# Kernel optimization log

Measured on AMD Instinct MI355X. Metric: run time of the kernel, lower is better.

The kernel has to match this reference:

```python
import jax, jax.numpy as jnp
import numpy as np

B, S, D, R = 2, 2048, 1024, 224  # batch, seq, n_embd, table_size


def setup_inputs() -> dict:
    key = jax.random.key(0)
    k = jax.random.split(key, 6)
    return {
        "hidden_states": jax.random.normal(k[0], (B, S, D), jnp.float32),
        "w_row": jax.random.normal(k[1], (D, R), jnp.float32) * 0.02,
        "b_row": jnp.zeros((R,), jnp.float32),
        "col_weight": jax.random.normal(k[2], (R, D, R), jnp.float32) * 0.02,
        "col_bias": jnp.zeros((R, R), jnp.float32),
        "target_row_ids": jax.random.randint(k[3], (B, S), 0, R, jnp.int32),
        "target_col_ids": jax.random.randint(k[4], (B, S), 0, R, jnp.int32),
    }


def reference(hidden_states, w_row, b_row, col_weight, col_bias,
              target_row_ids, target_col_ids):
    Bv, Sv, Dv = hidden_states.shape
    Rv = col_bias.shape[0]
    N = Bv * Sv
    hs_flat = hidden_states.reshape(N, Dv)
    r = target_row_ids.reshape(N)
    c = target_col_ids.reshape(N)

    # row loss: standard cross entropy over table_size row logits (mean)
    row_logits = hs_flat @ w_row + b_row                      # [N, R]
    logp_row = jax.nn.log_softmax(row_logits, axis=-1)
    loss_row = -jnp.take_along_axis(logp_row, r[:, None].astype(jnp.int32), axis=1)[:, 0].mean()

    # column loss: per-token row-routed projection + cross entropy (sum / N).
    # Mathematically identical to the original per-row masked loop: each token
    # uses col_weight[row_id] / col_bias[row_id]. We process tokens in fixed-size
    # chunks with lax.scan so FLOPs match the original (N*D*R, not N*R*D*R) and
    # the gathered per-token weights stay bounded in memory.
    CHUNK = 256  # N = 4096 divisible by CHUNK
    hs_c = hs_flat.reshape(N // CHUNK, CHUNK, Dv)
    r_c = r.reshape(N // CHUNK, CHUNK)
    c_c = c.reshape(N // CHUNK, CHUNK)

    def body(acc, xs):
        h, ri, ci = xs                          # [C,D], [C], [C]
        w = col_weight[ri]                      # [C, D, R] irregular gather
        b = col_bias[ri]                        # [C, R]
        logits = jnp.einsum('cd,cdk->ck', h, w) + b
        logp = jax.nn.log_softmax(logits, axis=-1)
        nll = -jnp.take_along_axis(logp, ci[:, None].astype(jnp.int32), axis=1)[:, 0]
        return acc + nll.sum(), None

    loss_col_sum, _ = jax.lax.scan(body, jnp.float32(0.0), (hs_c, r_c, c_c))
    loss_col = loss_col_sum / N
    return loss_row + loss_col
```

## Files before the change

kernel.cpp:

```cpp
#include <hip/hip_runtime.h>
#include <math.h>

#define D_DIM 1024
#define R_DIM 224
#define N_TOK 4096
#define KSPLIT 4
#define KRANGE (D_DIM / KSPLIT)
#define MCHUNK 32
#define NTHREADS 448
#define COL_GRID (R_DIM * KSPLIT)
#define ROW_MBLK (N_TOK / MCHUNK)
#define ROW_GRID (ROW_MBLK * KSPLIT)
#define GRID2 (COL_GRID + ROW_GRID)
#define L_FLOATS (N_TOK * R_DIM)

typedef short bf16x8 __attribute__((ext_vector_type(8)));
typedef short short8_t __attribute__((ext_vector_type(8)));
typedef float floatx4 __attribute__((ext_vector_type(4)));

__device__ __forceinline__ short f2bf(float f) {
    unsigned u = __float_as_uint(f);
    u += 0x7fffu + ((u >> 16) & 1u);
    return (short)(u >> 16);
}

__global__ __launch_bounds__(1024) void init_kernel(
    const int* __restrict__ rid, int* __restrict__ sorted,
    int* __restrict__ cnt, int* __restrict__ off,
    float* __restrict__ Lbuf, float* __restrict__ out)
{
    const int tid = threadIdx.x;
    if (blockIdx.x != 0) {
        const int zb = blockIdx.x - 1;
        float4* Lp = reinterpret_cast<float4*>(Lbuf);
        const int base = zb * 7168;
        for (int i = tid; i < 7168; i += 1024)
            Lp[base + i] = make_float4(0.f, 0.f, 0.f, 0.f);
        return;
    }
    __shared__ int h[256];
    __shared__ int sc[2][256];
    __shared__ int cur[R_DIM];
    if (tid < 256) h[tid] = 0;
    __syncthreads();
    for (int n = tid; n < N_TOK; n += 1024) atomicAdd(&h[rid[n]], 1);
    __syncthreads();
    if (tid < 256) sc[0][tid] = h[tid];
    __syncthreads();
    int src = 0;
    for (int d = 1; d < 256; d <<= 1) {
        if (tid < 256) {
            int v = sc[src][tid];
            if (tid >= d) v += sc[src][tid - d];
            sc[src ^ 1][tid] = v;
        }
        __syncthreads();
        src ^= 1;
    }
    if (tid < R_DIM) {
        int o = sc[src][tid] - h[tid];
        off[tid] = o;
        cnt[tid] = h[tid];
        cur[tid] = o;
    }
    if (tid == 0) out[0] = 0.0f;
    __syncthreads();
    for (int n = tid; n < N_TOK; n += 1024) {
        int p = atomicAdd(&cur[rid[n]], 1);
        sorted[p] = n;
    }
}

__global__ __launch_bounds__(NTHREADS) void gemm_kernel(
    const float* __restrict__ hs, const float* __restrict__ w_row,
    const float* __restrict__ w_col, const int* __restrict__ sorted,
    const int* __restrict__ cnt, const int* __restrict__ off,
    float* __restrict__ Lrow, float* __restrict__ Lcol)
{
    __shared__ short A_sh[MCHUNK * KRANGE];
    __shared__ int tok_sh[MCHUNK];

    const int bid = blockIdx.x;
    const int tid = threadIdx.x;
    const int lane = tid & 63;
    const int wv = tid >> 6;
    const int lm = lane & 15;
    const int lg = lane >> 4;

    const bool is_row = (bid >= COL_GRID);
    int ksp, tokbase, n_tok;
    const float* W;
    float* Ldst;
    if (is_row) {
        int idx = bid - COL_GRID;
        ksp = idx & 3;
        tokbase = (idx >> 2) * MCHUNK;
        n_tok = MCHUNK;
        W = w_row;
        Ldst = Lrow;
    } else {
        int rho = bid >> 2;
        ksp = bid & 3;
        tokbase = off[rho];
        n_tok = cnt[rho];
        W = w_col + (size_t)rho * D_DIM * R_DIM;
        Ldst = Lcol;
    }
    const int K0 = ksp * KRANGE;
    char* const Abp = (char*)A_sh;
    const int col0 = wv * 32 + lm;

    const int n_chunks = (n_tok + MCHUNK - 1) / MCHUNK;
    for (int p = 0; p < n_chunks; ++p) {
        __syncthreads();
        if (tid < MCHUNK) {
            int gi = p * MCHUNK + tid;
            tok_sh[tid] = (gi < n_tok)
                ? (is_row ? (tokbase + gi) : sorted[tokbase + gi]) : -1;
        }
        __syncthreads();
        for (int i = tid; i < MCHUNK * (KRANGE / 8); i += NTHREADS) {
            int row = i >> 5;
            int g8 = i & 31;
            int tok = tok_sh[row];
            float4 h0 = make_float4(0.f, 0.f, 0.f, 0.f);
            float4 h1 = make_float4(0.f, 0.f, 0.f, 0.f);
            if (tok >= 0) {
                const float* hp = &hs[(size_t)tok * D_DIM + K0 + g8 * 8];
                h0 = *reinterpret_cast<const float4*>(hp);
                h1 = *reinterpret_cast<const float4*>(hp + 4);
            }
            short8_t v = { f2bf(h0.x), f2bf(h0.y), f2bf(h0.z), f2bf(h0.w),
                           f2bf(h1.x), f2bf(h1.y), f2bf(h1.z), f2bf(h1.w) };
            *reinterpret_cast<short8_t*>(
                Abp + row * 512 + ((g8 * 16) ^ ((row & 7) << 4))) = v;
        }
        __syncthreads();

        floatx4 acc[2][2];
#pragma unroll
        for (int ms = 0; ms < 2; ++ms)
#pragma unroll
            for (int nt = 0; nt < 2; ++nt) acc[ms][nt] = (floatx4)0.0f;

        for (int ks = 0; ks < 8; ++ks) {
            const float* bp = W + (size_t)(K0 + ks * 32 + lg * 8) * R_DIM + col0;
            float braw0[8], braw1[8];
#pragma unroll
            for (int j = 0; j < 8; ++j) braw0[j] = bp[j * R_DIM];
#pragma unroll
            for (int j = 0; j < 8; ++j) braw1[j] = bp[j * R_DIM + 16];
            bf16x8 bf0 = { f2bf(braw0[0]), f2bf(braw0[1]), f2bf(braw0[2]), f2bf(braw0[3]),
                           f2bf(braw0[4]), f2bf(braw0[5]), f2bf(braw0[6]), f2bf(braw0[7]) };
            bf16x8 bf1 = { f2bf(braw1[0]), f2bf(braw1[1]), f2bf(braw1[2]), f2bf(braw1[3]),
                           f2bf(braw1[4]), f2bf(braw1[5]), f2bf(braw1[6]), f2bf(braw1[7]) };
            const int kbyte = ks * 64 + lg * 16;
#pragma unroll
            for (int ms = 0; ms < 2; ++ms) {
                int row = ms * 16 + lm;
                bf16x8 a = *reinterpret_cast<const bf16x8*>(
                    Abp + row * 512 + (kbyte ^ ((row & 7) << 4)));
                acc[ms][0] = __builtin_amdgcn_mfma_f32_16x16x32_bf16(a, bf0, acc[ms][0], 0, 0, 0);
                acc[ms][1] = __builtin_amdgcn_mfma_f32_16x16x32_bf16(a, bf1, acc[ms][1], 0, 0, 0);
            }
        }

#pragma unroll
        for (int ms = 0; ms < 2; ++ms)
#pragma unroll
            for (int r = 0; r < 4; ++r) {
                int mloc = ms * 16 + lg * 4 + r;
                int tok = tok_sh[mloc];
                if (tok >= 0) {
                    atomicAdd(&Ldst[(size_t)tok * R_DIM + col0], acc[ms][0][r]);
                    atomicAdd(&Ldst[(size_t)tok * R_DIM + col0 + 16], acc[ms][1][r]);
                }
            }
    }
}

__global__ __launch_bounds__(256) void loss_kernel(
    const float* __restrict__ Lrow, const float* __restrict__ Lcol,
    const float* __restrict__ b_row, const float* __restrict__ b_col,
    const int* __restrict__ rid, const int* __restrict__ cid,
    float* __restrict__ out)
{
    __shared__ float wsum[4];
    const int tid = threadIdx.x;
    const int lane = tid & 63;
    const int wv = tid >> 6;
    const int gw = blockIdx.x * 4 + wv;
    float accum = 0.0f;

    for (int n = gw; n < N_TOK; n += 512) {
        const int rt = rid[n];
        const int ct = cid[n];
#pragma unroll
        for (int part = 0; part < 2; ++part) {
            const float* Lp = (part == 0 ? Lrow : Lcol) + (size_t)n * R_DIM;
            const float* bp = (part == 0) ? b_row : (b_col + (size_t)rt * R_DIM);
            const int tgt = (part == 0) ? rt : ct;
            float v0 = Lp[lane] + bp[lane];
            float v1 = Lp[lane + 64] + bp[lane + 64];
            float v2 = Lp[lane + 128] + bp[lane + 128];
            float v3 = (lane < 32) ? (Lp[lane + 192] + bp[lane + 192]) : -1e30f;
            float m = fmaxf(fmaxf(v0, v1), fmaxf(v2, v3));
#pragma unroll
            for (int s = 32; s; s >>= 1) m = fmaxf(m, __shfl_xor(m, s));
            float sum = __expf(v0 - m) + __expf(v1 - m) + __expf(v2 - m)
                      + ((lane < 32) ? __expf(v3 - m) : 0.0f);
#pragma unroll
            for (int s = 32; s; s >>= 1) sum += __shfl_xor(sum, s);
            float tl = Lp[tgt] + bp[tgt];
            accum += -(tl - m - __logf(sum));
        }
    }
    if (lane == 0) wsum[wv] = accum;
    __syncthreads();
    if (tid == 0)
        atomicAdd(out, (wsum[0] + wsum[1] + wsum[2] + wsum[3]) * (1.0f / N_TOK));
}

extern "C" void kernel_launch(void* const* d_in, const int* in_sizes, int n_in,
                              void* d_out, int out_size, void* d_ws, size_t ws_size,
                              hipStream_t stream)
{
    const float* hs    = (const float*)d_in[0];
    const float* w_row = (const float*)d_in[1];
    const float* b_row = (const float*)d_in[2];
    const float* w_col = (const float*)d_in[3];
    const float* b_col = (const float*)d_in[4];
    const int* rid     = (const int*)d_in[5];
    const int* cid     = (const int*)d_in[6];
    float* out = (float*)d_out;

    float* Lrow = (float*)d_ws;
    float* Lcol = Lrow + L_FLOATS;
    int* sorted = (int*)(Lcol + L_FLOATS);
    int* cnt    = sorted + N_TOK;
    int* off    = cnt + R_DIM;

    hipLaunchKernelGGL(init_kernel, dim3(65), dim3(1024), 0, stream,
                       rid, sorted, cnt, off, Lrow, out);
    hipLaunchKernelGGL(gemm_kernel, dim3(GRID2), dim3(NTHREADS), 0, stream,
                       hs, w_row, w_col, sorted, cnt, off, Lrow, Lcol);
    hipLaunchKernelGGL(loss_kernel, dim3(128), dim3(256), 0, stream,
                       Lrow, Lcol, b_row, b_col, rid, cid, out);
}
```

Baseline: 338.4 us.

## Replace split-K atomic accumulation with per-split partial buffers reduced in loss kernel

Each K-split of the GEMM now writes its partial logits with plain stores into its own slice of an expanded workspace, instead of atomically adding into one shared buffer. The loss kernel then sums the four partial slices per token before the softmax. This removes the atomics and the zeroing pass in the init kernel, which now launches a single block. The cost is a workspace four times larger and four times more reads in the loss kernel.

```diff
diff --git a/kernel.cpp b/kernel.cpp
--- a/kernel.cpp
+++ b/kernel.cpp
@@ -26,18 +26,9 @@
 
 __global__ __launch_bounds__(1024) void init_kernel(
     const int* __restrict__ rid, int* __restrict__ sorted,
-    int* __restrict__ cnt, int* __restrict__ off,
-    float* __restrict__ Lbuf, float* __restrict__ out)
+    int* __restrict__ cnt, int* __restrict__ off, float* __restrict__ out)
 {
     const int tid = threadIdx.x;
-    if (blockIdx.x != 0) {
-        const int zb = blockIdx.x - 1;
-        float4* Lp = reinterpret_cast<float4*>(Lbuf);
-        const int base = zb * 7168;
-        for (int i = tid; i < 7168; i += 1024)
-            Lp[base + i] = make_float4(0.f, 0.f, 0.f, 0.f);
-        return;
-    }
     __shared__ int h[256];
     __shared__ int sc[2][256];
     __shared__ int cur[R_DIM];
@@ -75,7 +66,7 @@
     const float* __restrict__ hs, const float* __restrict__ w_row,
     const float* __restrict__ w_col, const int* __restrict__ sorted,
     const int* __restrict__ cnt, const int* __restrict__ off,
-    float* __restrict__ Lrow, float* __restrict__ Lcol)
+    float* __restrict__ Lrow_p, float* __restrict__ Lcol_p)
 {
     __shared__ short A_sh[MCHUNK * KRANGE];
     __shared__ int tok_sh[MCHUNK];
@@ -97,14 +88,14 @@
         tokbase = (idx >> 2) * MCHUNK;
         n_tok = MCHUNK;
         W = w_row;
-        Ldst = Lrow;
+        Ldst = Lrow_p + (size_t)ksp * L_FLOATS;
     } else {
         int rho = bid >> 2;
         ksp = bid & 3;
         tokbase = off[rho];
         n_tok = cnt[rho];
         W = w_col + (size_t)rho * D_DIM * R_DIM;
-        Ldst = Lcol;
+        Ldst = Lcol_p + (size_t)ksp * L_FLOATS;
     }
     const int K0 = ksp * KRANGE;
     char* const Abp = (char*)A_sh;
@@ -172,15 +163,15 @@
                 int mloc = ms * 16 + lg * 4 + r;
                 int tok = tok_sh[mloc];
                 if (tok >= 0) {
-                    atomicAdd(&Ldst[(size_t)tok * R_DIM + col0], acc[ms][0][r]);
-                    atomicAdd(&Ldst[(size_t)tok * R_DIM + col0 + 16], acc[ms][1][r]);
+                    Ldst[(size_t)tok * R_DIM + col0]      = acc[ms][0][r];
+                    Ldst[(size_t)tok * R_DIM + col0 + 16] = acc[ms][1][r];
                 }
             }
     }
 }
 
 __global__ __launch_bounds__(256) void loss_kernel(
-    const float* __restrict__ Lrow, const float* __restrict__ Lcol,
+    const float* __restrict__ Lrow_p, const float* __restrict__ Lcol_p,
     const float* __restrict__ b_row, const float* __restrict__ b_col,
     const int* __restrict__ rid, const int* __restrict__ cid,
     float* __restrict__ out)
@@ -197,13 +188,23 @@
         const int ct = cid[n];
 #pragma unroll
         for (int part = 0; part < 2; ++part) {
-            const float* Lp = (part == 0 ? Lrow : Lcol) + (size_t)n * R_DIM;
+            const float* Lbase = (part == 0 ? Lrow_p : Lcol_p) + (size_t)n * R_DIM;
             const float* bp = (part == 0) ? b_row : (b_col + (size_t)rt * R_DIM);
             const int tgt = (part == 0) ? rt : ct;
-            float v0 = Lp[lane] + bp[lane];
-            float v1 = Lp[lane + 64] + bp[lane + 64];
-            float v2 = Lp[lane + 128] + bp[lane + 128];
-            float v3 = (lane < 32) ? (Lp[lane + 192] + bp[lane + 192]) : -1e30f;
+            float v0 = 0.f, v1 = 0.f, v2 = 0.f, v3s = 0.f, vt = 0.f;
+#pragma unroll
+            for (int ksp = 0; ksp < KSPLIT; ++ksp) {
+                const float* Lp = Lbase + (size_t)ksp * L_FLOATS;
+                v0 += Lp[lane];
+                v1 += Lp[lane + 64];
+                v2 += Lp[lane + 128];
+                if (lane < 32) v3s += Lp[lane + 192];
+                vt += Lp[tgt];
+            }
+            v0 += bp[lane];
+            v1 += bp[lane + 64];
+            v2 += bp[lane + 128];
+            float v3 = (lane < 32) ? (v3s + bp[lane + 192]) : -1e30f;
             float m = fmaxf(fmaxf(v0, v1), fmaxf(v2, v3));
 #pragma unroll
             for (int s = 32; s; s >>= 1) m = fmaxf(m, __shfl_xor(m, s));
@@ -211,7 +212,7 @@
                       + ((lane < 32) ? __expf(v3 - m) : 0.0f);
 #pragma unroll
             for (int s = 32; s; s >>= 1) sum += __shfl_xor(sum, s);
-            float tl = Lp[tgt] + bp[tgt];
+            float tl = vt + bp[tgt];
             accum += -(tl - m - __logf(sum));
         }
     }
@@ -234,16 +235,16 @@
     const int* cid     = (const int*)d_in[6];
     float* out = (float*)d_out;
 
-    float* Lrow = (float*)d_ws;
-    float* Lcol = Lrow + L_FLOATS;
-    int* sorted = (int*)(Lcol + L_FLOATS);
+    float* Lrow_p = (float*)d_ws;
+    float* Lcol_p = Lrow_p + (size_t)KSPLIT * L_FLOATS;
+    int* sorted = (int*)(Lcol_p + (size_t)KSPLIT * L_FLOATS);
     int* cnt    = sorted + N_TOK;
     int* off    = cnt + R_DIM;
 
-    hipLaunchKernelGGL(init_kernel, dim3(65), dim3(1024), 0, stream,
-                       rid, sorted, cnt, off, Lrow, out);
+    hipLaunchKernelGGL(init_kernel, dim3(1), dim3(1024), 0, stream,
+                       rid, sorted, cnt, off, out);
     hipLaunchKernelGGL(gemm_kernel, dim3(GRID2), dim3(NTHREADS), 0, stream,
-                       hs, w_row, w_col, sorted, cnt, off, Lrow, Lcol);
+                       hs, w_row, w_col, sorted, cnt, off, Lrow_p, Lcol_p);
     hipLaunchKernelGGL(loss_kernel, dim3(128), dim3(256), 0, stream,
-                       Lrow, Lcol, b_row, b_col, rid, cid, out);
-}
+                       Lrow_p, Lcol_p, b_row, b_col, rid, cid, out);
+}
```

Result: slower. 350.0 us (+3.4%).
